# Optimization experiments

Measured on AMD Instinct MI355X. Metric: run time of the kernel, lower is better.

Reference implementation:

```python
import jax, jax.numpy as jnp
import numpy as np

N = 4096
REG_STRENGTH = 1.0
BLOCK_EPS = 1e-6  # tolerance for detecting pooled-block boundaries in the backward


@jax.custom_vjp
def isotonic_l2(y):
    """argmin_{v_1 >= v_2 >= ... >= v_n} 0.5 * ||v - y||^2 (PAV solution).

    Computed via the exact minimax characterization, fully vectorized:
        v_i = min_{j <= i} max_{k >= i} mean(y[j..k])
    """
    return _iso_solution(y)


def _iso_solution(y):
    n = y.shape[0]
    cs = jnp.concatenate([jnp.zeros((1,), y.dtype), jnp.cumsum(y)])  # [n+1]
    idx = jnp.arange(n)
    j = idx[:, None]  # block start
    k = idx[None, :]  # block end
    length = (k - j + 1).astype(y.dtype)
    A = (cs[k + 1] - cs[j]) / length            # mean(y[j..k]) where k >= j
    A = jnp.where(k >= j, A, -jnp.inf)
    # M[j, i] = max_{k >= i} A[j, k]  (reverse cumulative max along k)
    M = jnp.flip(jax.lax.cummax(jnp.flip(A, axis=1), axis=1), axis=1)
    # v_i = min_{j <= i} M[j, i]  (cumulative min along j, take diagonal)
    v = jnp.diagonal(jax.lax.cummin(M, axis=0))
    return v


def _iso_fwd(y):
    v = _iso_solution(y)
    return v, v


def _iso_bwd(v, g):
    # Jacobian of PAV: within each pooled block, grad is the block mean of g.
    n = v.shape[0]
    drop = (v[:-1] - v[1:]) > BLOCK_EPS * jnp.maximum(jnp.abs(v[:-1]), 1.0)
    bid = jnp.concatenate([jnp.zeros((1,), jnp.int32),
                           jnp.cumsum(drop.astype(jnp.int32))])
    sums = jax.ops.segment_sum(g, bid, num_segments=n)
    cnts = jax.ops.segment_sum(jnp.ones_like(g), bid, num_segments=n)
    return ((sums / jnp.maximum(cnts, 1.0))[bid],)


isotonic_l2.defvjp(_iso_fwd, _iso_bwd)


def soft_rank(x, regularization_strength):
    """torchsort-style L2 soft rank: project x/eps onto permutahedron P([n..1])."""
    n = x.shape[0]
    theta = x / regularization_strength
    perm = jnp.argsort(-theta)          # descending sort permutation (constant wrt grad)
    s = theta[perm]
    w = jnp.arange(n, 0, -1, dtype=x.dtype)  # [n, n-1, ..., 1]
    sol = isotonic_l2(s - w)
    ranks_sorted = s - sol
    inv = jnp.argsort(perm)
    return ranks_sorted[inv]


def setup_inputs() -> dict:
    key = jax.random.key(0)
    kp, kt = jax.random.split(key)
    pred = jax.random.normal(kp, (N,), dtype=jnp.float32)
    target = jax.random.normal(kt, (N,), dtype=jnp.float32)
    return {"pred": pred, "target": target}


def reference(pred, target):
    p = soft_rank(pred, REG_STRENGTH)
    t = soft_rank(target, REG_STRENGTH)
    p = p - p.mean()
    p = p / jnp.linalg.norm(p)
    t = t - t.mean()
    t = t / jnp.linalg.norm(t)
    return 1.0 - jnp.sum(p * t)
```

## Files before the change

kernel.cpp:

```cpp
#include <hip/hip_runtime.h>
#include <math.h>

#define NEL   4096
#define NT    1024
#define HALF  512
#define EPT   8
#define CPT   4
#define NPROD 128
#define JLEN  256
#define MAGICZ 0x13579BDFu
#define MAGICP 0x2468ACE1u

#define WSYNC() asm volatile("s_waitcnt lgkmcnt(0)" ::: "memory")

__device__ inline void pav_merge(double* P, int* C, const int lo, const int mid,
                                 const int hi) {
  const int llen = C[mid - 1];
  int cs = mid - llen;
  const int rlen = C[mid];
  int ce = mid + rlen - 1;
  const double mL = (P[mid] - P[cs]) / (double)llen;
  const double mR = (P[ce + 1] - P[mid]) / (double)rlen;
  if (mL <= mR) {
    double mu = (P[ce + 1] - P[cs]) / (double)(ce - cs + 1);
    bool changed = true;
    while (changed) {
      changed = false;
      while (cs > lo) {
        const int l2 = C[cs - 1];
        const double m2 = (P[cs] - P[cs - l2]) / (double)l2;
        if (m2 <= mu) {
          cs -= l2;
          mu = (P[ce + 1] - P[cs]) / (double)(ce - cs + 1);
          changed = true;
        } else break;
      }
      while (ce < hi - 1) {
        const int l2 = C[ce + 1];
        const double m2 = (P[ce + 1 + l2] - P[ce + 1]) / (double)l2;
        if (m2 >= mu) {
          ce += l2;
          mu = (P[ce + 1] - P[cs]) / (double)(ce - cs + 1);
          changed = true;
        } else break;
      }
    }
    const int len = ce - cs + 1;
    C[cs] = len;
    C[ce] = len;
  }
}

__global__ __launch_bounds__(NT, 1)
void spearman_kernel(const float* __restrict__ pred,
                     const float* __restrict__ target,
                     unsigned int* __restrict__ ws,
                     float* __restrict__ loss_out) {
  __shared__ float  s_val[2][NEL];
  __shared__ double s_P[2][NEL + 1];
  __shared__ int    s_cnt[2][NEL];
  __shared__ double s_wsum[2][HALF / 64];
  __shared__ int    s_nb[2];
  __shared__ double s_red[NT / 64][5];

  unsigned int* counts = ws;
  unsigned int* dflags = ws + 2 * NEL;
  unsigned int* zflag  = ws + 2 * NEL + NPROD;

  const int tid  = threadIdx.x;
  const int lane = tid & 63;
  const int wid  = tid >> 6;

  if (blockIdx.x != 0) {
    const int pid = blockIdx.x - 1;
    const int arr = pid >> 6;
    const int rem = pid & 63;
    const int ic  = rem >> 4;
    const int js  = rem & 15;
    const float* __restrict__ x = arr ? target : pred;
    const int i     = ic * NT + tid;
    const int jbase = js * JLEN;

    float* jv = s_val[0];
    if (tid < JLEN) jv[tid] = x[jbase + tid];
    const float xi = x[i];
    __syncthreads();

    unsigned int c = 0;
    const float4* jv4 = (const float4*)jv;
#pragma unroll 8
    for (int t4 = 0; t4 < JLEN / 4; t4++) {
      const float4 v = jv4[t4];
      const int j = jbase + 4 * t4;
      c += (v.x > xi || (v.x == xi && j + 0 < i)) ? 1u : 0u;
      c += (v.y > xi || (v.y == xi && j + 1 < i)) ? 1u : 0u;
      c += (v.z > xi || (v.z == xi && j + 2 < i)) ? 1u : 0u;
      c += (v.w > xi || (v.w == xi && j + 3 < i)) ? 1u : 0u;
    }
    while (__hip_atomic_load(zflag, __ATOMIC_ACQUIRE,
                             __HIP_MEMORY_SCOPE_AGENT) != MAGICZ)
      __builtin_amdgcn_s_sleep(1);
    atomicAdd(&counts[arr * NEL + i], c);
    __syncthreads();
    if (tid == 0) {
      __threadfence();
      __hip_atomic_store(&dflags[pid], MAGICP, __ATOMIC_RELEASE,
                         __HIP_MEMORY_SCOPE_AGENT);
    }
    return;
  }

  const float4 xp = ((const float4*)pred)[tid];
  const float4 xt = ((const float4*)target)[tid];
  counts[tid]       = 0u;
  counts[NT + tid]  = 0u;
  counts[2 * NT + tid] = 0u;
  counts[3 * NT + tid] = 0u;
  counts[4 * NT + tid] = 0u;
  counts[5 * NT + tid] = 0u;
  counts[6 * NT + tid] = 0u;
  counts[7 * NT + tid] = 0u;
  __syncthreads();
  if (tid == 0) {
    __threadfence();
    __hip_atomic_store(zflag, MAGICZ, __ATOMIC_RELEASE,
                       __HIP_MEMORY_SCOPE_AGENT);
  }
  if (tid < NPROD) {
    while (__hip_atomic_load(&dflags[tid], __ATOMIC_ACQUIRE,
                             __HIP_MEMORY_SCOPE_AGENT) != MAGICP)
      __builtin_amdgcn_s_sleep(1);
    __threadfence();
  }
  __syncthreads();

  int rp[CPT], rt[CPT];
  {
    const int4 a = ((const int4*)counts)[tid];
    const int4 b = ((const int4*)counts)[NEL / 4 + tid];
    rp[0] = a.x; rp[1] = a.y; rp[2] = a.z; rp[3] = a.w;
    rt[0] = b.x; rt[1] = b.y; rt[2] = b.z; rt[3] = b.w;
    s_val[0][rp[0]] = xp.x; s_val[0][rp[1]] = xp.y;
    s_val[0][rp[2]] = xp.z; s_val[0][rp[3]] = xp.w;
    s_val[1][rt[0]] = xt.x; s_val[1][rt[1]] = xt.y;
    s_val[1][rt[2]] = xt.z; s_val[1][rt[3]] = xt.w;
  }
  __syncthreads();

  const int arr = tid >> 9;
  const int tA  = tid & (HALF - 1);
  const int wA  = tA >> 6;
  const int b0  = tA * EPT;
  double* P = s_P[arr];
  int*    C = s_cnt[arr];

  double c[EPT];
  {
    double acc = 0.0;
#pragma unroll
    for (int e = 0; e < EPT; e++) {
      const int p = b0 + e;
      acc += (double)s_val[arr][p] - (double)(NEL - p);
      c[e] = acc;
    }
  }
  const double tot = c[EPT - 1];
  double sc = tot;
#pragma unroll
  for (int d = 1; d < 64; d <<= 1) {
    const double o = __shfl_up(sc, d, 64);
    if (lane >= d) sc += o;
  }
  if (lane == 63) s_wsum[arr][wA] = sc;
  __syncthreads();
  double wexcl = 0.0;
#pragma unroll
  for (int w = 0; w < HALF / 64; w++)
    wexcl += (w < wA) ? s_wsum[arr][w] : 0.0;
  const double excl = wexcl + (sc - tot);
#pragma unroll
  for (int e = 0; e < EPT; e++) P[b0 + 1 + e] = excl + c[e];
  if (lane == 0) P[b0] = excl;

  C[b0] = 1;
  for (int p = b0 + 1; p < b0 + EPT; p++) {
    int cs = p;
    const double Pe = P[p + 1];
    while (cs > b0) {
      const int l2 = C[cs - 1];
      const int lb = cs - l2;
      const double Pcs = P[cs];
      const double Plb = (lb == b0) ? excl : P[lb];
      const double mPrev = (Pcs - Plb) / (double)l2;
      const double mCur  = (Pe - Pcs) / (double)(p - cs + 1);
      if (mPrev <= mCur) cs = lb; else break;
    }
    C[cs] = p - cs + 1;
    C[p]  = p - cs + 1;
  }
  WSYNC();

  const int wbase = wA * 512;
#pragma unroll
  for (int m = EPT; m <= 256; m <<= 1) {
    const int nm = 512 / (2 * m);
    if (lane < nm) {
      const int lo = wbase + lane * 2 * m;
      pav_merge(P, C, lo, lo + m, lo + 2 * m);
    }
    WSYNC();
  }
  __syncthreads();

  if (wA == 0) {
#pragma unroll
    for (int m = 512; m <= 2048; m <<= 1) {
      const int nm = NEL / (2 * m);
      if (lane < nm) {
        const int lo = lane * 2 * m;
        pav_merge(P, C, lo, lo + m, lo + 2 * m);
      }
      WSYNC();
    }
    if (lane == 0) {
      int s = 0, b = 0;
      while (s < NEL) {
        const int cc = C[s];
        C[b] = s;
        b++;
        s += cc;
      }
      s_nb[arr] = b;
    }
  }
  __syncthreads();

  const int nb = s_nb[arr];
#pragma unroll
  for (int e = 0; e < EPT; e++) {
    const int p = b0 + e;
    int lo = 0, hi = nb - 1;
    while (lo < hi) {
      const int md = (lo + hi + 1) >> 1;
      if (C[md] <= p) lo = md; else hi = md - 1;
    }
    const int st = C[lo];
    const int en = (lo + 1 < nb) ? C[lo + 1] : NEL;
    const double v = (P[en] - P[st]) / (double)(en - st);
    s_val[arr][p] = (float)((double)s_val[arr][p] - v);
  }
  __syncthreads();

  double Sp = 0.0, Sq = 0.0, Spp = 0.0, Sqq = 0.0, Spq = 0.0;
#pragma unroll
  for (int e = 0; e < CPT; e++) {
    const double p = (double)s_val[0][rp[e]];
    const double q = (double)s_val[1][rt[e]];
    Sp += p; Sq += q; Spp += p * p; Sqq += q * q; Spq += p * q;
  }
#pragma unroll
  for (int d = 32; d > 0; d >>= 1) {
    Sp  += __shfl_down(Sp,  d, 64);
    Sq  += __shfl_down(Sq,  d, 64);
    Spp += __shfl_down(Spp, d, 64);
    Sqq += __shfl_down(Sqq, d, 64);
    Spq += __shfl_down(Spq, d, 64);
  }
  if (lane == 0) {
    s_red[wid][0] = Sp;  s_red[wid][1] = Sq;  s_red[wid][2] = Spp;
    s_red[wid][3] = Sqq; s_red[wid][4] = Spq;
  }
  __syncthreads();
  if (tid == 0) {
    double a0 = 0, a1 = 0, a2 = 0, a3 = 0, a4 = 0;
    for (int w = 0; w < NT / 64; w++) {
      a0 += s_red[w][0]; a1 += s_red[w][1]; a2 += s_red[w][2];
      a3 += s_red[w][3]; a4 += s_red[w][4];
    }
    const double n  = (double)NEL;
    const double mp = a0 / n, mq = a1 / n;
    const double cov = a4 - n * mp * mq;
    const double vp  = a2 - n * mp * mp;
    const double vq  = a3 - n * mq * mq;
    loss_out[0] = (float)(1.0 - cov / sqrt(vp * vq));
  }
}

extern "C" void kernel_launch(void* const* d_in, const int* in_sizes, int n_in,
                              void* d_out, int out_size, void* d_ws, size_t ws_size,
                              hipStream_t stream) {
  const float* pred   = (const float*)d_in[0];
  const float* target = (const float*)d_in[1];
  unsigned int* ws = (unsigned int*)d_ws;
  float* out = (float*)d_out;

  hipLaunchKernelGGL(spearman_kernel, dim3(NPROD + 1), dim3(NT), 0, stream,
                     pred, target, ws, out);
}
```

Measured before the change: 98.28 us.

## Halve block size, use done-counter sync, and division-free PAV comparisons

```diff
diff --git a/kernel.cpp b/kernel.cpp
--- a/kernel.cpp
+++ b/kernel.cpp
@@ -2,14 +2,15 @@
 #include <math.h>
 
 #define NEL   4096
-#define NT    1024
-#define HALF  512
-#define EPT   8
-#define CPT   4
-#define NPROD 128
+#define NT    512
+#define HALF  256
+#define EPT   16
+#define CPT   8
+#define NPROD 256
 #define JLEN  256
 #define MAGICZ 0x13579BDFu
-#define MAGICP 0x2468ACE1u
+#define DONE_W 8192
+#define ZFLG_W 8193
 
 #define WSYNC() asm volatile("s_waitcnt lgkmcnt(0)" ::: "memory")
 
@@ -19,29 +20,24 @@
   int cs = mid - llen;
   const int rlen = C[mid];
   int ce = mid + rlen - 1;
-  const double mL = (P[mid] - P[cs]) / (double)llen;
-  const double mR = (P[ce + 1] - P[mid]) / (double)rlen;
-  if (mL <= mR) {
-    double mu = (P[ce + 1] - P[cs]) / (double)(ce - cs + 1);
+  const double Pmid = P[mid];
+  double Pcs = P[cs], Pce1 = P[ce + 1];
+  if ((Pmid - Pcs) * (double)rlen <= (Pce1 - Pmid) * (double)llen) {
     bool changed = true;
     while (changed) {
       changed = false;
       while (cs > lo) {
         const int l2 = C[cs - 1];
-        const double m2 = (P[cs] - P[cs - l2]) / (double)l2;
-        if (m2 <= mu) {
-          cs -= l2;
-          mu = (P[ce + 1] - P[cs]) / (double)(ce - cs + 1);
-          changed = true;
+        const double Pl = P[cs - l2];
+        if ((Pcs - Pl) * (double)(ce - cs + 1) <= (Pce1 - Pcs) * (double)l2) {
+          cs -= l2; Pcs = Pl; changed = true;
         } else break;
       }
       while (ce < hi - 1) {
         const int l2 = C[ce + 1];
-        const double m2 = (P[ce + 1 + l2] - P[ce + 1]) / (double)l2;
-        if (m2 >= mu) {
-          ce += l2;
-          mu = (P[ce + 1] - P[cs]) / (double)(ce - cs + 1);
-          changed = true;
+        const double Pr = P[ce + 1 + l2];
+        if ((Pr - Pce1) * (double)(ce - cs + 1) >= (Pce1 - Pcs) * (double)l2) {
+          ce += l2; Pce1 = Pr; changed = true;
         } else break;
       }
     }
@@ -63,21 +59,17 @@
   __shared__ int    s_nb[2];
   __shared__ double s_red[NT / 64][5];
 
-  unsigned int* counts = ws;
-  unsigned int* dflags = ws + 2 * NEL;
-  unsigned int* zflag  = ws + 2 * NEL + NPROD;
-
   const int tid  = threadIdx.x;
   const int lane = tid & 63;
   const int wid  = tid >> 6;
 
   if (blockIdx.x != 0) {
     const int pid = blockIdx.x - 1;
-    const int arr = pid >> 6;
-    const int rem = pid & 63;
-    const int ic  = rem >> 4;
-    const int js  = rem & 15;
-    const float* __restrict__ x = arr ? target : pred;
+    const int parr = pid >> 7;
+    const int rem  = pid & 127;
+    const int ic   = rem >> 4;
+    const int js   = rem & 15;
+    const float* __restrict__ x = parr ? target : pred;
     const int i     = ic * NT + tid;
     const int jbase = js * JLEN;
 
@@ -97,57 +89,71 @@
       c += (v.z > xi || (v.z == xi && j + 2 < i)) ? 1u : 0u;
       c += (v.w > xi || (v.w == xi && j + 3 < i)) ? 1u : 0u;
     }
-    while (__hip_atomic_load(zflag, __ATOMIC_ACQUIRE,
-                             __HIP_MEMORY_SCOPE_AGENT) != MAGICZ)
-      __builtin_amdgcn_s_sleep(1);
-    atomicAdd(&counts[arr * NEL + i], c);
+    if (tid == 0) {
+      while (__hip_atomic_load(&ws[ZFLG_W], __ATOMIC_RELAXED,
+                               __HIP_MEMORY_SCOPE_AGENT) != MAGICZ)
+        __builtin_amdgcn_s_sleep(2);
+      (void)__hip_atomic_load(&ws[ZFLG_W], __ATOMIC_ACQUIRE,
+                              __HIP_MEMORY_SCOPE_AGENT);
+    }
     __syncthreads();
-    if (tid == 0) {
-      __threadfence();
-      __hip_atomic_store(&dflags[pid], MAGICP, __ATOMIC_RELEASE,
-                         __HIP_MEMORY_SCOPE_AGENT);
-    }
+    atomicAdd(&ws[parr * NEL + i], c);
+    __threadfence();
+    __syncthreads();
+    if (tid == 0)
+      __hip_atomic_fetch_add(&ws[DONE_W], 1u, __ATOMIC_RELEASE,
+                             __HIP_MEMORY_SCOPE_AGENT);
     return;
   }
 
-  const float4 xp = ((const float4*)pred)[tid];
-  const float4 xt = ((const float4*)target)[tid];
-  counts[tid]       = 0u;
-  counts[NT + tid]  = 0u;
-  counts[2 * NT + tid] = 0u;
-  counts[3 * NT + tid] = 0u;
-  counts[4 * NT + tid] = 0u;
-  counts[5 * NT + tid] = 0u;
-  counts[6 * NT + tid] = 0u;
-  counts[7 * NT + tid] = 0u;
+  const float4 xp0 = ((const float4*)pred)[2 * tid];
+  const float4 xp1 = ((const float4*)pred)[2 * tid + 1];
+  const float4 xt0 = ((const float4*)target)[2 * tid];
+  const float4 xt1 = ((const float4*)target)[2 * tid + 1];
+  {
+    const int4 z = make_int4(0, 0, 0, 0);
+    int4* w4 = (int4*)ws;
+    w4[tid] = z; w4[tid + 512] = z; w4[tid + 1024] = z; w4[tid + 1536] = z;
+    if (tid == 0) ws[DONE_W] = 0u;
+  }
   __syncthreads();
   if (tid == 0) {
     __threadfence();
-    __hip_atomic_store(zflag, MAGICZ, __ATOMIC_RELEASE,
+    __hip_atomic_store(&ws[ZFLG_W], MAGICZ, __ATOMIC_RELEASE,
                        __HIP_MEMORY_SCOPE_AGENT);
-  }
-  if (tid < NPROD) {
-    while (__hip_atomic_load(&dflags[tid], __ATOMIC_ACQUIRE,
-                             __HIP_MEMORY_SCOPE_AGENT) != MAGICP)
-      __builtin_amdgcn_s_sleep(1);
-    __threadfence();
+    unsigned int v;
+    do {
+      __builtin_amdgcn_s_sleep(2);
+      v = __hip_atomic_load(&ws[DONE_W], __ATOMIC_RELAXED,
+                            __HIP_MEMORY_SCOPE_AGENT);
+    } while (v != NPROD);
+    (void)__hip_atomic_load(&ws[DONE_W], __ATOMIC_ACQUIRE,
+                            __HIP_MEMORY_SCOPE_AGENT);
   }
   __syncthreads();
 
   int rp[CPT], rt[CPT];
   {
-    const int4 a = ((const int4*)counts)[tid];
-    const int4 b = ((const int4*)counts)[NEL / 4 + tid];
-    rp[0] = a.x; rp[1] = a.y; rp[2] = a.z; rp[3] = a.w;
-    rt[0] = b.x; rt[1] = b.y; rt[2] = b.z; rt[3] = b.w;
-    s_val[0][rp[0]] = xp.x; s_val[0][rp[1]] = xp.y;
-    s_val[0][rp[2]] = xp.z; s_val[0][rp[3]] = xp.w;
-    s_val[1][rt[0]] = xt.x; s_val[1][rt[1]] = xt.y;
-    s_val[1][rt[2]] = xt.z; s_val[1][rt[3]] = xt.w;
-  }
-  __syncthreads();
-
-  const int arr = tid >> 9;
+    const int4 a0 = ((const int4*)ws)[2 * tid];
+    const int4 a1 = ((const int4*)ws)[2 * tid + 1];
+    const int4 b0_ = ((const int4*)ws)[NEL / 4 + 2 * tid];
+    const int4 b1_ = ((const int4*)ws)[NEL / 4 + 2 * tid + 1];
+    rp[0] = a0.x; rp[1] = a0.y; rp[2] = a0.z; rp[3] = a0.w;
+    rp[4] = a1.x; rp[5] = a1.y; rp[6] = a1.z; rp[7] = a1.w;
+    rt[0] = b0_.x; rt[1] = b0_.y; rt[2] = b0_.z; rt[3] = b0_.w;
+    rt[4] = b1_.x; rt[5] = b1_.y; rt[6] = b1_.z; rt[7] = b1_.w;
+    s_val[0][rp[0]] = xp0.x; s_val[0][rp[1]] = xp0.y;
+    s_val[0][rp[2]] = xp0.z; s_val[0][rp[3]] = xp0.w;
+    s_val[0][rp[4]] = xp1.x; s_val[0][rp[5]] = xp1.y;
+    s_val[0][rp[6]] = xp1.z; s_val[0][rp[7]] = xp1.w;
+    s_val[1][rt[0]] = xt0.x; s_val[1][rt[1]] = xt0.y;
+    s_val[1][rt[2]] = xt0.z; s_val[1][rt[3]] = xt0.w;
+    s_val[1][rt[4]] = xt1.x; s_val[1][rt[5]] = xt1.y;
+    s_val[1][rt[6]] = xt1.z; s_val[1][rt[7]] = xt1.w;
+  }
+  __syncthreads();
+
+  const int arr = tid >> 8;
   const int tA  = tid & (HALF - 1);
   const int wA  = tA >> 6;
   const int b0  = tA * EPT;
@@ -191,19 +197,19 @@
       const int lb = cs - l2;
       const double Pcs = P[cs];
       const double Plb = (lb == b0) ? excl : P[lb];
-      const double mPrev = (Pcs - Plb) / (double)l2;
-      const double mCur  = (Pe - Pcs) / (double)(p - cs + 1);
-      if (mPrev <= mCur) cs = lb; else break;
+      if ((Pcs - Plb) * (double)(p - cs + 1) <= (Pe - Pcs) * (double)l2)
+        cs = lb;
+      else break;
     }
     C[cs] = p - cs + 1;
     C[p]  = p - cs + 1;
   }
   WSYNC();
 
-  const int wbase = wA * 512;
-#pragma unroll
-  for (int m = EPT; m <= 256; m <<= 1) {
-    const int nm = 512 / (2 * m);
+  const int wbase = wA * 1024;
+#pragma unroll
+  for (int m = EPT; m <= 512; m <<= 1) {
+    const int nm = 1024 / (2 * m);
     if (lane < nm) {
       const int lo = wbase + lane * 2 * m;
       pav_merge(P, C, lo, lo + m, lo + 2 * m);
@@ -214,7 +220,7 @@
 
   if (wA == 0) {
 #pragma unroll
-    for (int m = 512; m <= 2048; m <<= 1) {
+    for (int m = 1024; m <= 2048; m <<= 1) {
       const int nm = NEL / (2 * m);
       if (lane < nm) {
         const int lo = lane * 2 * m;
```

Measured after the change: 120.2 us. 22.3% more time.
